# Kernel optimization log

Hardware: AMD Instinct MI355X
Metric: run time of the kernel (lower is better)

## Reference

```python
import jax, jax.numpy as jnp
import numpy as np

BETA = 0.25
N_EMBED = 1024
DIM = 256


def setup_inputs() -> dict:
    key = jax.random.key(0)
    k1, k2 = jax.random.split(key)
    z = jax.random.normal(k1, (8, DIM, 64, 64), dtype=jnp.float32)
    # matches nn.Embedding init: uniform(-1/n_embed, 1/n_embed)
    codebook = jax.random.uniform(
        k2, (N_EMBED, DIM), dtype=jnp.float32,
        minval=-1.0 / N_EMBED, maxval=1.0 / N_EMBED)
    return {"z": z, "codebook": codebook}


def reference(z, codebook):
    B, C, H, W = z.shape
    sg = jax.lax.stop_gradient
    zp = jnp.transpose(z, (0, 2, 3, 1))          # [B,H,W,C]
    zf = zp.reshape(-1, C)                        # [N,C], N = B*H*W
    # squared euclidean distances: ||z||^2 + ||e||^2 - 2 z.e
    d = (jnp.sum(zf * zf, axis=1, keepdims=True)
         + jnp.sum(codebook * codebook, axis=1)
         - 2.0 * zf @ codebook.T)                 # [N, n_embed]
    idx = jnp.argmin(d, axis=1)                   # [N]
    # one-hot @ codebook in the original is just an index gather
    z_q = codebook[idx].reshape(zp.shape)         # [B,H,W,C]
    loss = (BETA * jnp.mean((sg(z_q) - zp) ** 2)
            + jnp.mean((z_q - sg(zp)) ** 2))
    z_q_st = zp + sg(z_q - zp)                    # straight-through estimator
    z_q_out = jnp.transpose(z_q_st, (0, 3, 1, 2))  # back to NCHW
    return z_q_out, loss, idx.reshape(B, H, W)
```

## Files before the change

kernel.cpp:

```cpp
#include <hip/hip_runtime.h>
#include <hip/hip_fp16.h>

#define NELEM 8388608
#define M_GAP 6e-4f
#define SCORE_SCALE (-1.0f / 512.0f)

typedef _Float16 f16x8 __attribute__((ext_vector_type(8)));
typedef short s16x8 __attribute__((ext_vector_type(8)));
typedef float f32x4 __attribute__((ext_vector_type(4)));

__device__ __forceinline__ unsigned short bf16r(float f) {
  unsigned u = __float_as_uint(f);
  return (unsigned short)((u + 0x7fffu + ((u >> 16) & 1u)) >> 16);
}
__device__ __forceinline__ float bf16f(unsigned short h) {
  return __uint_as_float(((unsigned)h) << 16);
}

__device__ __forceinline__ float pw128_sq(const float* p, int s) {
  float r[8];
#pragma unroll
  for (int j = 0; j < 8; ++j) { float v = p[j * s]; r[j] = __fmul_rn(v, v); }
#pragma unroll
  for (int i = 8; i < 128; i += 8) {
#pragma unroll
    for (int j = 0; j < 8; ++j) {
      float v = p[(i + j) * s];
      r[j] = __fadd_rn(r[j], __fmul_rn(v, v));
    }
  }
  return __fadd_rn(__fadd_rn(__fadd_rn(r[0], r[1]), __fadd_rn(r[2], r[3])),
                   __fadd_rn(__fadd_rn(r[4], r[5]), __fadd_rn(r[6], r[7])));
}
__device__ __forceinline__ float np_sumsq256(const float* p, int s) {
  return __fadd_rn(pw128_sq(p, s), pw128_sq(p + 128 * s, s));
}

__global__ __launch_bounds__(256)
void vq_prep(const float* __restrict__ cb, unsigned short* __restrict__ cbimg,
             float* __restrict__ cbT, float* __restrict__ Bsg,
             unsigned* __restrict__ cnt, float* __restrict__ loss) {
  __shared__ float rows[16][260];
  const int t = threadIdx.x;
  const int b = blockIdx.x;
  if (b == 0 && t == 0) { cnt[0] = 0u; *loss = 0.0f; }
#pragma unroll
  for (int i = 0; i < 4; ++i) {
    int idx = t + i * 256;
    int r = idx >> 6, c4 = idx & 63;
    float4 v = reinterpret_cast<const float4*>(cb + (size_t)(b * 16 + r) * 256)[c4];
    rows[r][c4 * 4 + 0] = v.x;
    rows[r][c4 * 4 + 1] = v.y;
    rows[r][c4 * 4 + 2] = v.z;
    rows[r][c4 * 4 + 3] = v.w;
  }
  __syncthreads();
  if (t < 16) Bsg[b * 16 + t] = np_sumsq256(&rows[t][0], 1);
#pragma unroll
  for (int uu = 0; uu < 2; ++uu) {
    int u = t * 2 + uu;
    int kk = u >> 6, rem = u & 63;
    int lk = rem >> 4, jj = rem & 15;
    int c0 = kk * 32 + lk * 8;
    s16x8 hv;
#pragma unroll
    for (int m = 0; m < 8; ++m)
      hv[m] = (short)__half_as_ushort(__float2half(rows[jj][c0 + m] * 1024.0f));
    *reinterpret_cast<s16x8*>(cbimg + (size_t)b * 4096 + u * 8) = hv;
  }
  {
    float* dst = cbT + (size_t)t * 1024 + b * 16;
#pragma unroll
    for (int jj = 0; jj < 16; ++jj) dst[jj] = rows[jj][t];
  }
}

#define VQ_STEP_PF(IT2, DO_PF)                                                 \
  {                                                                            \
    f32x4 acc[2];                                                              \
    acc[0] = (f32x4){0.f, 0.f, 0.f, 0.f};                                      \
    acc[1] = (f32x4){0.f, 0.f, 0.f, 0.f};                                      \
    _Pragma("unroll")                                                          \
    for (int kk = 0; kk < 8; ++kk) {                                           \
      f16x8 bcur = ba[kk];                                                     \
      if (DO_PF)                                                               \
        ba[kk] = cimg2[(size_t)(wv * 16 + (IT2) + 1) * 512 + kk * 64 + lane];  \
      _Pragma("unroll")                                                        \
      for (int rs = 0; rs < 2; ++rs)                                           \
        acc[rs] = __builtin_amdgcn_mfma_f32_16x16x32_f16(ah[rs][kk], bcur,     \
                                                         acc[rs], 0, 0, 0);    \
    }                                                                          \
    int j = wv * 256 + (IT2) * 16 + l15;                                       \
    float Bj = BsL[j];                                                         \
    _Pragma("unroll")                                                          \
    for (int rs = 0; rs < 2; ++rs) {                                           \
      _Pragma("unroll")                                                        \
      for (int r = 0; r < 4; ++r) {                                            \
        float s = fmaf(SCORE_SCALE, acc[rs][r], Bj);                           \
        bool lt = s < b1v[rs][r];                                              \
        float other = lt ? b1v[rs][r] : s;                                     \
        b2v[rs][r] = fminf(b2v[rs][r], other);                                 \
        b1v[rs][r] = fminf(b1v[rs][r], s);                                     \
        b1i[rs][r] = lt ? j : b1i[rs][r];                                      \
      }                                                                        \
    }                                                                          \
  }

__global__ __launch_bounds__(256, 1)
void vq_fast(const float* __restrict__ z, const float* __restrict__ cb,
             const unsigned short* __restrict__ cbimg,
             const float* __restrict__ Bsg,
             float* __restrict__ zq, float* __restrict__ loss,
             float* __restrict__ idxo,
             unsigned* __restrict__ list, unsigned* __restrict__ cnt,
             float* __restrict__ zdump) {
  __shared__ __align__(16) unsigned char buf[33792];
  __shared__ float BsL[1024];
  __shared__ float part[32][33];
  __shared__ float rowA[32];
  __shared__ int bestj[32];
  __shared__ float bestd[32];
  __shared__ unsigned char flg[32];
  __shared__ float wred[4];
  __shared__ float cv1[4 * 32], cv2[4 * 32];
  __shared__ int ci1[4 * 32];

  const int t = threadIdx.x;
  const int bid = blockIdx.x;
  const int lane = t & 63;
  const int wv = t >> 6;
  const int l15 = lane & 15;
  const int lk = lane >> 4;
  const int bh = bid >> 1, half = bid & 1;

  const f16x8* cimg2 = reinterpret_cast<const f16x8*>(cbimg);
  float* zt = reinterpret_cast<float*>(buf);
  const float4* z4 = reinterpret_cast<const float4*>(
      z + (size_t)(bh >> 6) * 1048576 + (size_t)(bh & 63) * 64 + half * 32);

  f16x8 ba[8];
#pragma unroll
  for (int kk = 0; kk < 8; ++kk)
    ba[kk] = cimg2[(size_t)(wv * 16) * 512 + kk * 64 + lane];

  for (int i = t; i < 1024; i += 256) BsL[i] = Bsg[i];

  {
    float sq[4] = {0.f, 0.f, 0.f, 0.f};
#pragma unroll
    for (int i = 0; i < 8; ++i) {
      int idx = t + i * 256;
      int c = idx >> 3, w4p = idx & 7;
      float4 v = z4[(size_t)c * 1024 + w4p];
      zt[c * 33 + w4p * 4 + 0] = v.x;
      zt[c * 33 + w4p * 4 + 1] = v.y;
      zt[c * 33 + w4p * 4 + 2] = v.z;
      zt[c * 33 + w4p * 4 + 3] = v.w;
      sq[0] += v.x * v.x; sq[1] += v.y * v.y;
      sq[2] += v.z * v.z; sq[3] += v.w * v.w;
    }
#pragma unroll
    for (int q = 0; q < 4; ++q) part[t >> 3][(t & 7) * 4 + q] = sq[q];
  }
  __syncthreads();
  if (t < 32) {
    float s = 0.f;
#pragma unroll
    for (int g = 0; g < 32; ++g) s += part[g][t];
    rowA[t] = s;
  }

  f16x8 ah[2][8];
#pragma unroll
  for (int rs = 0; rs < 2; ++rs)
#pragma unroll
    for (int kk = 0; kk < 8; ++kk)
#pragma unroll
      for (int m = 0; m < 8; ++m)
        ah[rs][kk][m] = (_Float16)zt[(kk * 32 + lk * 8 + m) * 33 + rs * 16 + l15];
  __syncthreads();

  float b1v[2][4], b2v[2][4];
  int b1i[2][4];
#pragma unroll
  for (int rs = 0; rs < 2; ++rs)
#pragma unroll
    for (int r = 0; r < 4; ++r) { b1v[rs][r] = 3.4e38f; b2v[rs][r] = 3.4e38f; b1i[rs][r] = 0; }

  for (int it = 0; it < 15; ++it) {
    VQ_STEP_PF(it, true);
  }
  VQ_STEP_PF(15, false);

#pragma unroll
  for (int mk = 1; mk < 16; mk <<= 1) {
#pragma unroll
    for (int rs = 0; rs < 2; ++rs)
#pragma unroll
      for (int r = 0; r < 4; ++r) {
        float ov1 = __shfl_xor(b1v[rs][r], mk, 64);
        float ov2 = __shfl_xor(b2v[rs][r], mk, 64);
        int oi1 = __shfl_xor(b1i[rs][r], mk, 64);
        bool lt = ov1 < b1v[rs][r];
        float hi = lt ? b1v[rs][r] : ov1;
        b2v[rs][r] = fminf(fminf(b2v[rs][r], ov2), hi);
        b1v[rs][r] = fminf(b1v[rs][r], ov1);
        b1i[rs][r] = lt ? oi1 : b1i[rs][r];
      }
  }
  if (l15 == 0) {
#pragma unroll
    for (int rs = 0; rs < 2; ++rs)
#pragma unroll
      for (int r = 0; r < 4; ++r) {
        int rr = rs * 16 + lk * 4 + r;
        cv1[wv * 32 + rr] = b1v[rs][r];
        cv2[wv * 32 + rr] = b2v[rs][r];
        ci1[wv * 32 + rr] = b1i[rs][r];
      }
  }
  __syncthreads();

  if (t < 32) {
    float v1 = cv1[t], v2 = cv2[t];
    int i1 = ci1[t];
#pragma unroll
    for (int w = 1; w < 4; ++w) {
      float u1 = cv1[w * 32 + t], u2 = cv2[w * 32 + t];
      int ui = ci1[w * 32 + t];
      if (u1 < v1) { v2 = fminf(v1, u2); v1 = u1; i1 = ui; }
      else v2 = fminf(v2, u1);
    }
    bestj[t] = i1;
    bestd[t] = v1;
    flg[t] = (v2 - v1 <= M_GAP) ? 1 : 0;
    int n = bid * 32 + t;
    idxo[n] = (float)i1;
    if (flg[t]) { unsigned pos = atomicAdd(cnt, 1u); list[pos] = (unsigned)n; }
  }
  __syncthreads();

  for (int rr = 0; rr < 32; ++rr) {
    if (flg[rr])
      zdump[((size_t)bid * 32 + rr) * 256 + t] = zt[t * 33 + rr];
  }

  {
    float lv = (t < 32) ? (rowA[t] + bestd[t]) : 0.f;
#pragma unroll
    for (int off = 32; off > 0; off >>= 1) lv += __shfl_down(lv, off, 64);
    if (lane == 0) wred[wv] = lv;
  }
  __syncthreads();
  if (t == 0)
    atomicAdd(loss, (wred[0] + wred[1] + wred[2] + wred[3]) * (1.25f / (float)NELEM));
  __syncthreads();

  f32x4* ldsF4 = reinterpret_cast<f32x4*>(buf);
  const float* ldsF = reinterpret_cast<const float*>(buf);
  const float4* cb4 = reinterpret_cast<const float4*>(cb);
  float* zqb = zq + (size_t)(bh >> 6) * 1048576 + (size_t)(bh & 63) * 64 + half * 32;
#pragma unroll
  for (int i = 0; i < 8; ++i) {
    int item = t + i * 256;
    int rr = item >> 6, cc = item & 63;
    float4 v = cb4[(size_t)bestj[rr] * 64 + cc];
    ldsF4[rr * 64 + (cc ^ ((rr >> 2) & 7))] = (f32x4){v.x, v.y, v.z, v.w};
  }
  __syncthreads();
#pragma unroll
  for (int i = 0; i < 8; ++i) {
    int item = t + i * 256;
    int w4p = item & 7, c = item >> 3;
    float ov[4];
#pragma unroll
    for (int q = 0; q < 4; ++q) {
      int rr = w4p * 4 + q;
      ov[q] = ldsF[(rr * 64 + ((c >> 2) ^ ((rr >> 2) & 7))) * 4 + (c & 3)];
    }
    *reinterpret_cast<float4*>(zqb + (size_t)c * 4096 + w4p * 4) =
        make_float4(ov[0], ov[1], ov[2], ov[3]);
  }
}

__global__ __launch_bounds__(256)
void vq_exact_fast(const float* __restrict__ zdump, const float* __restrict__ cbT,
                   const float* __restrict__ Bsg, const unsigned* __restrict__ list,
                   const unsigned* __restrict__ cnt, float* __restrict__ idxo) {
  __shared__ float zr[8][260];
  __shared__ float Anp[8];
  __shared__ float rv[256];
  __shared__ int ri[256];
  const int t = threadIdx.x;
  const unsigned K = *cnt;
  const float4* cbT4 = reinterpret_cast<const float4*>(cbT);
  const float4* zd4 = reinterpret_cast<const float4*>(zdump);

  for (unsigned g = blockIdx.x; g * 8 < K; g += gridDim.x) {
    int nrows = (int)min(8u, K - g * 8);
    __syncthreads();
#pragma unroll
    for (int i = 0; i < 2; ++i) {
      int idx = t + i * 256;
      int r = idx >> 6, c4 = idx & 63;
      if (r < nrows) {
        float4 v = zd4[(size_t)list[g * 8 + r] * 64 + c4];
        zr[r][c4 * 4 + 0] = v.x; zr[r][c4 * 4 + 1] = v.y;
        zr[r][c4 * 4 + 2] = v.z; zr[r][c4 * 4 + 3] = v.w;
      }
    }
    __syncthreads();
    if (t < nrows) Anp[t] = np_sumsq256(&zr[t][0], 1);
    __syncthreads();

    float acc[8][4];
#pragma unroll
    for (int r = 0; r < 8; ++r)
#pragma unroll
      for (int q = 0; q < 4; ++q) acc[r][q] = 0.f;
    for (int c = 0; c < 256; ++c) {
      float4 bv = cbT4[c * 256 + t];
#pragma unroll
      for (int r = 0; r < 8; ++r) {
        float zc = zr[r][c];
        acc[r][0] = fmaf(zc, bv.x, acc[r][0]);
        acc[r][1] = fmaf(zc, bv.y, acc[r][1]);
        acc[r][2] = fmaf(zc, bv.z, acc[r][2]);
        acc[r][3] = fmaf(zc, bv.w, acc[r][3]);
      }
    }
    for (int r = 0; r < nrows; ++r) {
      float A = Anp[r];
      float bvv = 3.4e38f;
      int bii = 0;
#pragma unroll
      for (int q = 0; q < 4; ++q) {
        int j = t * 4 + q;
        float dd = __fsub_rn(__fadd_rn(A, Bsg[j]), __fmul_rn(2.0f, acc[r][q]));
        if (dd < bvv) { bvv = dd; bii = j; }
      }
      rv[t] = bvv; ri[t] = bii;
      __syncthreads();
      for (int s2 = 128; s2 > 0; s2 >>= 1) {
        if (t < s2) {
          float v2 = rv[t + s2]; int i2 = ri[t + s2];
          if (v2 < rv[t] || (v2 == rv[t] && i2 < ri[t])) { rv[t] = v2; ri[t] = i2; }
        }
        __syncthreads();
      }
      if (t == 0) idxo[list[g * 8 + r]] = (float)ri[0];
      __syncthreads();
    }
  }
}

__global__ __launch_bounds__(256)
void vq_ref(const float* __restrict__ z, const float* __restrict__ cb,
            float* __restrict__ zq, float* __restrict__ loss,
            float* __restrict__ idxo) {
  __shared__ __align__(16) float zt[256 * 64];
  __shared__ __align__(16) float cbt[256 * 64];
  __shared__ float As[64];
  __shared__ float Bs[64];
  __shared__ int bestj[64];
  __shared__ float cand_v[16 * 64];
  __shared__ int cand_i[16 * 64];
  __shared__ double wred[4];
  const int t = threadIdx.x;
  const int wg = t & 15, jg = t >> 4;
  const int bid = blockIdx.x;
  const int b = bid >> 6, h = bid & 63;
  const int n0 = bid * 64;
  const float4* z4 = reinterpret_cast<const float4*>(z + (size_t)b * 256 * 4096 + (size_t)h * 64);
  float4* zt4 = reinterpret_cast<float4*>(zt);
#pragma unroll
  for (int i = 0; i < 16; ++i) {
    int idx4 = t + i * 256;
    zt4[idx4] = z4[(size_t)(idx4 >> 4) * 1024 + (idx4 & 15)];
  }
  __syncthreads();
  if (t < 64) As[t] = np_sumsq256(zt + t, 64);
  float bv[4]; int bi[4];
#pragma unroll
  for (int a = 0; a < 4; ++a) { bv[a] = 3.4e38f; bi[a] = 0; }
  for (int p = 0; p < 16; ++p) {
    __syncthreads();
    const float4* cb4 = reinterpret_cast<const float4*>(cb) + (size_t)p * 64 * 64;
#pragma unroll
    for (int i = 0; i < 16; ++i) {
      int idx4 = t + i * 256;
      int jj = idx4 >> 6, c4 = idx4 & 63;
      float4 v = cb4[idx4];
      cbt[(c4 * 4 + 0) * 64 + jj] = v.x;
      cbt[(c4 * 4 + 1) * 64 + jj] = v.y;
      cbt[(c4 * 4 + 2) * 64 + jj] = v.z;
      cbt[(c4 * 4 + 3) * 64 + jj] = v.w;
    }
    __syncthreads();
    if (t < 64) Bs[t] = np_sumsq256(cbt + t, 64);
    float acc[4][4];
#pragma unroll
    for (int a = 0; a < 4; ++a)
#pragma unroll
      for (int u = 0; u < 4; ++u) acc[a][u] = 0.0f;
    const float4* ztp = reinterpret_cast<const float4*>(zt) + wg;
    const float4* cbp = reinterpret_cast<const float4*>(cbt) + jg;
#pragma unroll 4
    for (int c = 0; c < 256; ++c) {
      float4 zv = ztp[c * 16];
      float4 cv = cbp[c * 16];
      float za[4] = {zv.x, zv.y, zv.z, zv.w};
      float ca[4] = {cv.x, cv.y, cv.z, cv.w};
#pragma unroll
      for (int a = 0; a < 4; ++a)
#pragma unroll
        for (int u = 0; u < 4; ++u) acc[a][u] = fmaf(za[a], ca[u], acc[a][u]);
    }
    __syncthreads();
#pragma unroll
    for (int u = 0; u < 4; ++u) {
      int j = p * 64 + jg * 4 + u;
      float Bju = Bs[jg * 4 + u];
#pragma unroll
      for (int a = 0; a < 4; ++a) {
        float AB = __fadd_rn(As[wg * 4 + a], Bju);
        float dd = __fsub_rn(AB, __fmul_rn(2.0f, acc[a][u]));
        if (dd < bv[a]) { bv[a] = dd; bi[a] = j; }
      }
    }
  }
  __syncthreads();
#pragma unroll
  for (int a = 0; a < 4; ++a) {
    int w = wg * 4 + a;
    cand_v[jg * 64 + w] = bv[a];
    cand_i[jg * 64 + w] = bi[a];
  }
  __syncthreads();
  if (t < 64) {
    float v0 = cand_v[t]; int i0 = cand_i[t];
    for (int g = 1; g < 16; ++g) {
      float v = cand_v[g * 64 + t]; int ii = cand_i[g * 64 + t];
      if (v < v0 || (v == v0 && ii < i0)) { v0 = v; i0 = ii; }
    }
    bestj[t] = i0;
    idxo[n0 + t] = (float)i0;
  }
  __syncthreads();
  double lsum = 0.0;
  float* zqbase = zq + (size_t)b * 256 * 4096 + (size_t)h * 64;
  for (int i = 0; i < 64; ++i) {
    int idx = t + i * 256;
    int c = idx >> 6, w = idx & 63;
    float zvv = zt[c * 64 + w];
    float cvv = cb[(size_t)bestj[w] * 256 + c];
    zqbase[(size_t)c * 4096 + w] = cvv;
    double d = (double)cvv - (double)zvv;
    lsum += d * d;
  }
#pragma unroll
  for (int off = 32; off > 0; off >>= 1) lsum += __shfl_down(lsum, off, 64);
  if ((t & 63) == 0) wred[t >> 6] = lsum;
  __syncthreads();
  if (t == 0) {
    double tot = wred[0] + wred[1] + wred[2] + wred[3];
    atomicAdd(loss, (float)(tot * (1.25 / (double)NELEM)));
  }
}

extern "C" void kernel_launch(void* const* d_in, const int* in_sizes, int n_in,
                              void* d_out, int out_size, void* d_ws, size_t ws_size,
                              hipStream_t stream) {
  (void)in_sizes; (void)n_in; (void)out_size;
  const float* z = (const float*)d_in[0];
  const float* cb = (const float*)d_in[1];
  float* out = (float*)d_out;
  float* zq = out;
  float* loss = out + NELEM;
  float* idxo = out + NELEM + 1;
  if (ws_size < 35651584) {
    hipMemsetAsync(loss, 0, sizeof(float), stream);
    vq_ref<<<512, 256, 0, stream>>>(z, cb, zq, loss, idxo);
    return;
  }
  unsigned char* ws = (unsigned char*)d_ws;
  unsigned* cnt = (unsigned*)ws;
  float* Bsg = (float*)(ws + 1024);
  unsigned* list = (unsigned*)(ws + 8192);
  float* cbT = (float*)(ws + 139264);
  unsigned short* cbimg = (unsigned short*)(ws + 1187840);
  float* zdump = (float*)(ws + 2097152);
  vq_prep<<<64, 256, 0, stream>>>(cb, cbimg, cbT, Bsg, cnt, loss);
  vq_fast<<<1024, 256, 0, stream>>>(z, cb, cbimg, Bsg, zq, loss, idxo, list, cnt, zdump);
  vq_exact_fast<<<512, 256, 0, stream>>>(zdump, cbT, Bsg, list, cnt, idxo);
}
```

Measured before the change: 96.81 us.

## Prefetch codebook tiles and batch argmin reduction across rows with shuffles

In the exact-fallback kernel, codebook loads are software-pipelined: eight float4 columns are prefetched one group ahead so global latency overlaps the FMA work. The per-row shared-memory tree argmin, which needed about nine barriers per row, is replaced by a single barrier after all eight rows write their partial minima. A 32-lane group per row then finishes the reduction with xor shuffles. This cuts synchronisation cost but uses more shared memory and registers. Rows beyond nrows are now reduced too but never written out.

```diff
diff --git a/kernel.cpp b/kernel.cpp
--- a/kernel.cpp
+++ b/kernel.cpp
@@ -289,8 +289,8 @@
                    const unsigned* __restrict__ cnt, float* __restrict__ idxo) {
   __shared__ float zr[8][260];
   __shared__ float Anp[8];
-  __shared__ float rv[256];
-  __shared__ int ri[256];
+  __shared__ float rvs[8][256];
+  __shared__ int ris[8][256];
   const int t = threadIdx.x;
   const unsigned K = *cnt;
   const float4* cbT4 = reinterpret_cast<const float4*>(cbT);
@@ -318,18 +318,39 @@
     for (int r = 0; r < 8; ++r)
 #pragma unroll
       for (int q = 0; q < 4; ++q) acc[r][q] = 0.f;
-    for (int c = 0; c < 256; ++c) {
-      float4 bv = cbT4[c * 256 + t];
-#pragma unroll
-      for (int r = 0; r < 8; ++r) {
-        float zc = zr[r][c];
-        acc[r][0] = fmaf(zc, bv.x, acc[r][0]);
-        acc[r][1] = fmaf(zc, bv.y, acc[r][1]);
-        acc[r][2] = fmaf(zc, bv.z, acc[r][2]);
-        acc[r][3] = fmaf(zc, bv.w, acc[r][3]);
-      }
-    }
-    for (int r = 0; r < nrows; ++r) {
+    float4 pre0, pre1, pre2, pre3, pre4, pre5, pre6, pre7;
+    pre0 = cbT4[0 * 256 + t]; pre1 = cbT4[1 * 256 + t];
+    pre2 = cbT4[2 * 256 + t]; pre3 = cbT4[3 * 256 + t];
+    pre4 = cbT4[4 * 256 + t]; pre5 = cbT4[5 * 256 + t];
+    pre6 = cbT4[6 * 256 + t]; pre7 = cbT4[7 * 256 + t];
+    for (int cg = 0; cg < 256; cg += 8) {
+      float4 cur0 = pre0, cur1 = pre1, cur2 = pre2, cur3 = pre3;
+      float4 cur4 = pre4, cur5 = pre5, cur6 = pre6, cur7 = pre7;
+      if (cg + 8 < 256) {
+        pre0 = cbT4[(cg + 8) * 256 + t];  pre1 = cbT4[(cg + 9) * 256 + t];
+        pre2 = cbT4[(cg + 10) * 256 + t]; pre3 = cbT4[(cg + 11) * 256 + t];
+        pre4 = cbT4[(cg + 12) * 256 + t]; pre5 = cbT4[(cg + 13) * 256 + t];
+        pre6 = cbT4[(cg + 14) * 256 + t]; pre7 = cbT4[(cg + 15) * 256 + t];
+      }
+#define EX_FMA(CUR, CI)                                                        \
+      {                                                                        \
+        float4 bv = CUR;                                                       \
+        _Pragma("unroll")                                                      \
+        for (int r = 0; r < 8; ++r) {                                          \
+          float zc = zr[r][cg + (CI)];                                         \
+          acc[r][0] = fmaf(zc, bv.x, acc[r][0]);                               \
+          acc[r][1] = fmaf(zc, bv.y, acc[r][1]);                               \
+          acc[r][2] = fmaf(zc, bv.z, acc[r][2]);                               \
+          acc[r][3] = fmaf(zc, bv.w, acc[r][3]);                               \
+        }                                                                      \
+      }
+      EX_FMA(cur0, 0) EX_FMA(cur1, 1) EX_FMA(cur2, 2) EX_FMA(cur3, 3)
+      EX_FMA(cur4, 4) EX_FMA(cur5, 5) EX_FMA(cur6, 6) EX_FMA(cur7, 7)
+#undef EX_FMA
+    }
+
+#pragma unroll
+    for (int r = 0; r < 8; ++r) {
       float A = Anp[r];
       float bvv = 3.4e38f;
       int bii = 0;
@@ -339,17 +360,26 @@
         float dd = __fsub_rn(__fadd_rn(A, Bsg[j]), __fmul_rn(2.0f, acc[r][q]));
         if (dd < bvv) { bvv = dd; bii = j; }
       }
-      rv[t] = bvv; ri[t] = bii;
-      __syncthreads();
-      for (int s2 = 128; s2 > 0; s2 >>= 1) {
-        if (t < s2) {
-          float v2 = rv[t + s2]; int i2 = ri[t + s2];
-          if (v2 < rv[t] || (v2 == rv[t] && i2 < ri[t])) { rv[t] = v2; ri[t] = i2; }
+      rvs[r][t] = bvv; ris[r][t] = bii;
+    }
+    __syncthreads();
+
+    {
+      int r = t >> 5, s = t & 31;
+      if (r < nrows) {
+        float v0 = rvs[r][s]; int i0 = ris[r][s];
+#pragma unroll
+        for (int k = 1; k < 8; ++k) {
+          float v = rvs[r][s + 32 * k]; int ii = ris[r][s + 32 * k];
+          if (v < v0 || (v == v0 && ii < i0)) { v0 = v; i0 = ii; }
         }
-        __syncthreads();
-      }
-      if (t == 0) idxo[list[g * 8 + r]] = (float)ri[0];
-      __syncthreads();
+#pragma unroll
+        for (int mk = 1; mk < 32; mk <<= 1) {
+          float v = __shfl_xor(v0, mk, 32); int ii = __shfl_xor(i0, mk, 32);
+          if (v < v0 || (v == v0 && ii < i0)) { v0 = v; i0 = ii; }
+        }
+        if (s == 0) idxo[list[g * 8 + r]] = (float)i0;
+      }
     }
   }
 }
```

Measured after the change: 105.2 us. 1.09x slower.
